# Performance work log

Measured on AMD Instinct MI355X. Metric: run time of the kernel, lower is better.

Reference implementation:

```python
import jax, jax.numpy as jnp
import numpy as np

N = 100000      # nodes
E = 1000000     # edges
D_IN = 64       # in_channels
HID = 64        # hid_channels
ENC = 64        # encoding_dim
OUT = 2         # out_channels (classes)
EDGE_DIM = 32   # TimeEncode dim == edge_dim
HEADS = 2
HD = HID // 2   # per-head channels (32)


def _p(k, shape):
    s = 1.0 / np.sqrt(shape[0])
    return jax.random.uniform(k, shape, jnp.float32, -s, s)


def setup_inputs() -> dict:
    key = jax.random.key(0)
    ks = jax.random.split(key, 40)
    inp = {
        "x": jax.random.normal(ks[0], (N, D_IN), jnp.float32),
        "edge_index": jax.random.randint(ks[1], (2, E), 0, N),
        "node_time": jax.random.uniform(ks[2], (N,), jnp.float32) * 100.0,
        "edge_time": jax.random.uniform(ks[3], (E, 1), jnp.float32) * 100.0,
        "node_mean_out_time_interval": jax.random.uniform(ks[4], (N,), jnp.float32) * 10.0,
        "node_out_degree": jax.random.uniform(ks[5], (N,), jnp.float32) * 50.0,
        "y": jax.random.randint(ks[6], (N,), 0, OUT),
        "train_mask": jnp.ones((N,), bool),
        # TimeEncode: cos(t W + b)
        "time_w": _p(ks[7], (1, EDGE_DIM)), "time_b": jnp.zeros((EDGE_DIM,), jnp.float32),
        # TemporalFrequencyEncoder / DegreeEncoder: Linear(1, ENC)
        "tf_w": _p(ks[8], (1, ENC)), "tf_b": jnp.zeros((ENC,), jnp.float32),
        "deg_w": _p(ks[9], (1, ENC)), "deg_b": jnp.zeros((ENC,), jnp.float32),
        # lin: Linear(in, hid)
        "lin_w": _p(ks[10], (D_IN, HID)), "lin_b": jnp.zeros((HID,), jnp.float32),
        # TransformerConv projections (heads*HD = HID)
        "Wq": _p(ks[11], (HID, HEADS * HD)), "bq": jnp.zeros((HEADS * HD,), jnp.float32),
        "Wk": _p(ks[12], (HID, HEADS * HD)), "bk": jnp.zeros((HEADS * HD,), jnp.float32),
        "Wv": _p(ks[13], (HID, HEADS * HD)), "bv": jnp.zeros((HEADS * HD,), jnp.float32),
        "We": _p(ks[14], (EDGE_DIM, HEADS * HD)), "be": jnp.zeros((HEADS * HD,), jnp.float32),
        "Wskip": _p(ks[15], (HID, HEADS * HD)), "bskip": jnp.zeros((HEADS * HD,), jnp.float32),
        # size-2 context attention
        "wenc_w": _p(ks[16], (ENC, ENC)), "wenc_b": jnp.zeros((ENC,), jnp.float32),
        "wx_w": _p(ks[17], (HID, ENC)), "wx_b": jnp.zeros((ENC,), jnp.float32),
        # lin_combine: Linear(hid+enc, hid)
        "comb_w": _p(ks[18], (HID + ENC, HID)), "comb_b": jnp.zeros((HID,), jnp.float32),
        # out: Linear(hid, out)
        "out_w": _p(ks[19], (HID, OUT)), "out_b": jnp.zeros((OUT,), jnp.float32),
    }
    return inp


def reference(x, edge_index, node_time, edge_time, node_mean_out_time_interval,
              node_out_degree, y, train_mask,
              time_w, time_b, tf_w, tf_b, deg_w, deg_b, lin_w, lin_b,
              Wq, bq, Wk, bk, Wv, bv, We, be, Wskip, bskip,
              wenc_w, wenc_b, wx_w, wx_b, comb_w, comb_b, out_w, out_b):
    src, dst = edge_index[0], edge_index[1]

    # relative edge time -> TimeEncode (cos features), used as edge_attr [E, 32]
    rel_t = node_time[src][:, None] - edge_time          # [E,1]
    rel_t_enc = jnp.cos(rel_t @ time_w + time_b)         # [E,EDGE_DIM]

    h = jax.nn.relu(x @ lin_w + lin_b)                   # [N,HID] (dropout = identity, eval)

    # TransformerConv (PyG math): per-edge attention + scatter-softmax aggregate
    q = (h @ Wq + bq).reshape(N, HEADS, HD)[dst]          # [E,H,HD]
    e = (rel_t_enc @ We + be).reshape(E, HEADS, HD)       # [E,H,HD]
    k = (h @ Wk + bk).reshape(N, HEADS, HD)[src] + e
    v = (h @ Wv + bv).reshape(N, HEADS, HD)[src] + e
    alpha = (q * k).sum(-1) / np.float32(np.sqrt(HD))     # [E,H]
    m = jax.ops.segment_max(alpha, dst, num_segments=N)   # stable softmax per dst node
    ea = jnp.exp(alpha - m[dst])
    denom = jax.ops.segment_sum(ea, dst, num_segments=N)
    a = ea / (denom[dst] + 1e-16)
    agg = jax.ops.segment_sum(a[:, :, None] * v, dst, num_segments=N)
    h1 = agg.reshape(N, HEADS * HD) + h @ Wskip + bskip   # concat heads + root skip

    # size-2 context attention over (temporal-frequency, degree) encodings
    tf_enc = node_mean_out_time_interval[:, None] @ tf_w + tf_b   # [N,ENC]
    deg_enc = node_out_degree[:, None] @ deg_w + deg_b            # [N,ENC]
    enc = jnp.stack((tf_enc, deg_enc), axis=1)                    # [N,2,ENC]
    enc_proj = jnp.tanh(enc @ wenc_w + wenc_b)                    # [N,2,ENC]
    x_proj = jnp.tanh(h1 @ wx_w + wx_b)                           # [N,ENC]
    score = jax.nn.softmax(jnp.einsum('nkd,nd->nk', enc_proj, x_proj), axis=1)  # [N,2]
    context = enc[:, 0] * score[:, 0:1] + enc[:, 1] * score[:, 1:2]

    h1 = jnp.concatenate((h1, context), axis=1) @ comb_w + comb_b  # [N,HID]
    logp = jax.nn.log_softmax(h1 @ out_w + out_b, axis=1)          # [N,OUT]
    return (h1, logp, y, train_mask)
```

## Files before the change

kernel.cpp:

```cpp
#include <hip/hip_runtime.h>
#include <hip/hip_fp16.h>

#define DEV __device__ __forceinline__

typedef _Float16 f16x8 __attribute__((ext_vector_type(8)));
typedef float f32x4 __attribute__((ext_vector_type(4)));

DEV float mask_val(const unsigned char* mb, int n) {
  unsigned b0 = mb[0], b1 = mb[1], b2 = mb[2], b3 = mb[3];
  if (b0 <= 1u && b1 == b0 && b2 == b0 && b3 == b0) {
    return mb[n] ? 1.f : 0.f;
  } else if (b1 == 0u && b2 == 0u && b3 == 0u) {
    return ((const int*)mb)[n] ? 1.f : 0.f;
  } else {
    return (((const float*)mb)[n] != 0.f) ? 1.f : 0.f;
  }
}

DEV float head_sum32(float x) {
  x += __int_as_float(__builtin_amdgcn_ds_swizzle(__float_as_int(x), 0x041F));
  x += __int_as_float(__builtin_amdgcn_ds_swizzle(__float_as_int(x), 0x081F));
  x += __int_as_float(__builtin_amdgcn_ds_swizzle(__float_as_int(x), 0x101F));
  x += __int_as_float(__builtin_amdgcn_ds_swizzle(__float_as_int(x), 0x201F));
  x += __int_as_float(__builtin_amdgcn_ds_swizzle(__float_as_int(x), 0x401F));
  return x;
}

__global__ void k_precompute(const float* __restrict__ tf_w, const float* __restrict__ tf_b,
                             const float* __restrict__ deg_w, const float* __restrict__ deg_b,
                             const float* __restrict__ wenc_w, const float* __restrict__ wenc_b,
                             const float* __restrict__ comb_w, float* __restrict__ cbuf) {
  int c = threadIdx.x;
  float A0 = 0, B0 = 0, A1 = 0, B1 = 0, P0 = 0, Q0 = 0, P1 = 0, Q1 = 0;
  for (int j = 0; j < 64; ++j) {
    float w  = wenc_w[j * 64 + c];
    float cw = comb_w[(64 + j) * 64 + c];
    float twj = tf_w[j], tbj = tf_b[j], dwj = deg_w[j], dbj = deg_b[j];
    A0 += twj * w;  B0 += tbj * w;
    A1 += dwj * w;  B1 += dbj * w;
    P0 += twj * cw; Q0 += tbj * cw;
    P1 += dwj * cw; Q1 += dbj * cw;
  }
  float wb = wenc_b[c];
  cbuf[c]       = A0; cbuf[64 + c]  = B0 + wb;
  cbuf[128 + c] = A1; cbuf[192 + c] = B1 + wb;
  cbuf[256 + c] = P0; cbuf[320 + c] = Q0;
  cbuf[384 + c] = P1; cbuf[448 + c] = Q1;
}

__global__ __launch_bounds__(256) void k_wcvt(
    const float* __restrict__ lin_w, const float* __restrict__ Wq,
    const float* __restrict__ Wk, const float* __restrict__ Wv,
    const float* __restrict__ Wsk, _Float16* __restrict__ wt) {
  const float* Ws[5] = {lin_w, Wq, Wk, Wv, Wsk};
  int idx = blockIdx.x * 256 + threadIdx.x;
  if (idx < 5 * 4096) {
    int s = idx >> 12, r = idx & 4095;
    int j = r >> 6, c = r & 63;
    wt[(s << 12) + c * 64 + j] = (_Float16)Ws[s][j * 64 + c];
  }
}

__global__ __launch_bounds__(256) void k_node_proj(
    const float* __restrict__ x, const _Float16* __restrict__ wt,
    const float* __restrict__ lin_b, const float* __restrict__ bq,
    const float* __restrict__ bk, const float* __restrict__ bv,
    const float* __restrict__ bsk, const float* __restrict__ be,
    float* __restrict__ q, __half2* __restrict__ kvp,
    float* __restrict__ skipout, int N) {
  __shared__ _Float16 H[4][16 * 72];
  const int tid = threadIdx.x;
  const int lane = tid & 63;
  const int wv = tid >> 6;
  const int mrow = lane & 15;
  const int kgrp = lane >> 4;
  const float invs = 0.17677669529663687f;
  float b_lin[4], b_q[4], b_k[4], b_v[4], b_sk[4];
#pragma unroll
  for (int nt = 0; nt < 4; ++nt) {
    const int cc = nt * 16 + mrow;
    b_lin[nt] = lin_b[cc];
    b_q[nt] = bq[cc];
    b_k[nt] = bk[cc] + be[cc];
    b_v[nt] = bv[cc] + be[cc];
    b_sk[nt] = bsk[cc];
  }
  _Float16* Hw = H[wv];
  const int ntiles = (N + 63) >> 6;
  for (int tile = blockIdx.x; tile < ntiles; tile += gridDim.x) {
    const int base = tile << 6;
    const int rowA = base + wv * 16 + mrow;
    const int rclamp = (rowA < N) ? rowA : (N - 1);
    const float* xr = x + (size_t)rclamp * 64 + kgrp * 8;
    const float4 u0 = *(const float4*)xr;
    const float4 u1 = *(const float4*)(xr + 4);
    const float4 u2 = *(const float4*)(xr + 32);
    const float4 u3 = *(const float4*)(xr + 36);
    const f16x8 a0 = {(_Float16)u0.x, (_Float16)u0.y, (_Float16)u0.z, (_Float16)u0.w,
                      (_Float16)u1.x, (_Float16)u1.y, (_Float16)u1.z, (_Float16)u1.w};
    const f16x8 a1 = {(_Float16)u2.x, (_Float16)u2.y, (_Float16)u2.z, (_Float16)u2.w,
                      (_Float16)u3.x, (_Float16)u3.y, (_Float16)u3.z, (_Float16)u3.w};
#pragma unroll
    for (int nt = 0; nt < 4; ++nt) {
      const _Float16* wb0 = wt + (nt * 16 + mrow) * 64 + kgrp * 8;
      const f16x8 B0 = *(const f16x8*)wb0;
      const f16x8 B1 = *(const f16x8*)(wb0 + 32);
      f32x4 C = {0.f, 0.f, 0.f, 0.f};
      C = __builtin_amdgcn_mfma_f32_16x16x32_f16(a0, B0, C, 0, 0, 0);
      C = __builtin_amdgcn_mfma_f32_16x16x32_f16(a1, B1, C, 0, 0, 0);
#pragma unroll
      for (int r = 0; r < 4; ++r) {
        const float hval = fmaxf(C[r] + b_lin[nt], 0.f);
        Hw[(kgrp * 4 + r) * 72 + nt * 16 + mrow] = (_Float16)hval;
      }
    }
    const f16x8 ha0 = *(const f16x8*)(Hw + mrow * 72 + kgrp * 8);
    const f16x8 ha1 = *(const f16x8*)(Hw + mrow * 72 + 32 + kgrp * 8);
    const int orow0 = base + wv * 16 + kgrp * 4;
#pragma unroll
    for (int nt = 0; nt < 4; ++nt) {
      const _Float16* wb0 = wt + 4096 + (nt * 16 + mrow) * 64 + kgrp * 8;
      const f16x8 B0 = *(const f16x8*)wb0;
      const f16x8 B1 = *(const f16x8*)(wb0 + 32);
      f32x4 C = {0.f, 0.f, 0.f, 0.f};
      C = __builtin_amdgcn_mfma_f32_16x16x32_f16(ha0, B0, C, 0, 0, 0);
      C = __builtin_amdgcn_mfma_f32_16x16x32_f16(ha1, B1, C, 0, 0, 0);
#pragma unroll
      for (int r = 0; r < 4; ++r) {
        const int orow = orow0 + r;
        if (orow < N) q[(size_t)orow * 64 + nt * 16 + mrow] = (C[r] + b_q[nt]) * invs;
      }
    }
#pragma unroll
    for (int nt = 0; nt < 4; ++nt) {
      const _Float16* wk0 = wt + 2 * 4096 + (nt * 16 + mrow) * 64 + kgrp * 8;
      const _Float16* wv0 = wt + 3 * 4096 + (nt * 16 + mrow) * 64 + kgrp * 8;
      const f16x8 Bk0 = *(const f16x8*)wk0;
      const f16x8 Bk1 = *(const f16x8*)(wk0 + 32);
      const f16x8 Bv0 = *(const f16x8*)wv0;
      const f16x8 Bv1 = *(const f16x8*)(wv0 + 32);
      f32x4 Ck = {0.f, 0.f, 0.f, 0.f};
      f32x4 Cv = {0.f, 0.f, 0.f, 0.f};
      Ck = __builtin_amdgcn_mfma_f32_16x16x32_f16(ha0, Bk0, Ck, 0, 0, 0);
      Ck = __builtin_amdgcn_mfma_f32_16x16x32_f16(ha1, Bk1, Ck, 0, 0, 0);
      Cv = __builtin_amdgcn_mfma_f32_16x16x32_f16(ha0, Bv0, Cv, 0, 0, 0);
      Cv = __builtin_amdgcn_mfma_f32_16x16x32_f16(ha1, Bv1, Cv, 0, 0, 0);
#pragma unroll
      for (int r = 0; r < 4; ++r) {
        const int orow = orow0 + r;
        if (orow < N)
          kvp[(size_t)orow * 64 + nt * 16 + mrow] =
              __halves2half2(__float2half_rn(Ck[r] + b_k[nt]), __float2half_rn(Cv[r] + b_v[nt]));
      }
    }
#pragma unroll
    for (int nt = 0; nt < 4; ++nt) {
      const _Float16* wb0 = wt + 4 * 4096 + (nt * 16 + mrow) * 64 + kgrp * 8;
      const f16x8 B0 = *(const f16x8*)wb0;
      const f16x8 B1 = *(const f16x8*)(wb0 + 32);
      f32x4 C = {0.f, 0.f, 0.f, 0.f};
      C = __builtin_amdgcn_mfma_f32_16x16x32_f16(ha0, B0, C, 0, 0, 0);
      C = __builtin_amdgcn_mfma_f32_16x16x32_f16(ha1, B1, C, 0, 0, 0);
#pragma unroll
      for (int r = 0; r < 4; ++r) {
        const int orow = orow0 + r;
        if (orow < N) skipout[(size_t)orow * 64 + nt * 16 + mrow] = C[r] + b_sk[nt];
      }
    }
  }
}

__global__ __launch_bounds__(256) void k_hist(const int* __restrict__ ei, int* __restrict__ counts, int E) {
  int i = blockIdx.x * 256 + threadIdx.x;
  if (i < E) atomicAdd(&counts[ei[E + i]], 1);
}

__global__ __launch_bounds__(256) void k_scan1(const int* __restrict__ counts, int* __restrict__ excl,
                                               int* __restrict__ bsum, int N) {
  __shared__ int s[256];
  const int t = threadIdx.x;
  const int idx = blockIdx.x * 256 + t;
  int val = (idx < N) ? counts[idx] : 0;
  s[t] = val;
  __syncthreads();
  for (int d = 1; d < 256; d <<= 1) {
    int add = (t >= d) ? s[t - d] : 0;
    __syncthreads();
    s[t] += add;
    __syncthreads();
  }
  if (idx < N) excl[idx] = s[t] - val;
  if (t == 255) bsum[blockIdx.x] = s[255];
}

__global__ __launch_bounds__(1024) void k_scan2(int* __restrict__ bsum, int B) {
  __shared__ int sm[1024];
  const int t = threadIdx.x;
  if (B <= 1024) {
    int val = (t < B) ? bsum[t] : 0;
    sm[t] = val;
    __syncthreads();
    for (int d = 1; d < 1024; d <<= 1) {
      int add = (t >= d) ? sm[t - d] : 0;
      __syncthreads();
      sm[t] += add;
      __syncthreads();
    }
    if (t < B) bsum[t] = sm[t] - val;
  } else if (t == 0) {
    int acc = 0;
    for (int i = 0; i < B; ++i) { int tt = bsum[i]; bsum[i] = acc; acc += tt; }
  }
}

__global__ __launch_bounds__(256) void k_scan3(const int* __restrict__ bsum, int* __restrict__ rowptr,
                                               int* __restrict__ next, int N, int E) {
  int i = blockIdx.x * 256 + threadIdx.x;
  if (i < N) {
    int r = rowptr[i] + bsum[i >> 8];
    rowptr[i] = r;
    next[i] = r;
  }
  if (i == 0) rowptr[N] = E;
}

__global__ __launch_bounds__(256) void k_fill(const int* __restrict__ ei,
                                              const float* __restrict__ node_time,
                                              const float* __restrict__ edge_time,
                                              int* __restrict__ next, int2* __restrict__ er, int E) {
  int e = blockIdx.x * 256 + threadIdx.x;
  if (e < E) {
    int s = ei[e], d = ei[E + e];
    int pos = atomicAdd(&next[d], 1);
    er[pos] = make_int2(s, __float_as_int(node_time[s] - edge_time[e]));
  }
}

__global__ __launch_bounds__(256) void k_aggregate(
    const int* __restrict__ rowptr, const int2* __restrict__ er,
    const float* __restrict__ q, const unsigned* __restrict__ kvu,
    const float* __restrict__ time_w, const float* __restrict__ time_b,
    const float* __restrict__ We,
    float* __restrict__ h1, int N) {
  __shared__ float swS[4][64];
  const int tid = threadIdx.x;
  const int c = tid & 63;
  const int wv = tid >> 6;
  const float INV2PI = 0.15915494309189535f;
  float wcol[32], Gw[32];
#pragma unroll
  for (int j = 0; j < 32; ++j) wcol[j] = We[j * 64 + c];
#pragma unroll
  for (int j = 0; j < 32; ++j) Gw[j] = We[(c & 31) * 64 + (c & 32) + j];
  const float tw = time_w[c & 31] * INV2PI;
  const float tb = time_b[c & 31] * INV2PI;
  const int h32 = c & 32;
  const int n0 = blockIdx.x * 4 + wv;
  const int nstride = gridDim.x * 4;
  for (int n = n0; n < N; n += nstride) {
    const int start = rowptr[n];
    const int end = rowptr[n + 1];
    const float qc = q[(size_t)n * 64 + c];
    swS[wv][c] = qc;
    float Gc = 0.f;
#pragma unroll
    for (int j = 0; j < 32; ++j) Gc = fmaf(swS[wv][h32 | j], Gw[j], Gc);
    float m = -1e30f, den = 0.f, num = 0.f, S = 0.f;
    for (int ce = start; ce < end; ce += 16) {
      const int cnt = (end - ce < 16) ? (end - ce) : 16;
      int src_[16];
      float rr_[16];
#pragma unroll
      for (int i = 0; i < 16; ++i) {
        const int ee = ce + ((i < cnt) ? i : cnt - 1);
        const int2 a = er[ee];
        src_[i] = a.x;
        rr_[i] = __int_as_float(a.y);
      }
      unsigned kvr[16];
#pragma unroll
      for (int i = 0; i < 16; ++i) kvr[i] = kvu[(size_t)src_[i] * 64 + c];
      float rv_[16], p[16];
#pragma unroll
      for (int i = 0; i < 16; ++i) {
        float ang = fmaf(rr_[i], tw, tb);
        ang = ang - floorf(ang);
        rv_[i] = __builtin_amdgcn_cosf(ang);
        const __half2 h2 = *(const __half2*)&kvr[i];
        p[i] = fmaf(rv_[i], Gc, qc * __half2float(h2.x));
      }
#pragma unroll
      for (int i = 0; i < 16; ++i) p[i] = head_sum32(p[i]);
#pragma unroll
      for (int i = 0; i < 16; ++i)
        if (i >= cnt) p[i] = -1e30f;
      float cm = p[0];
#pragma unroll
      for (int i = 1; i < 16; ++i) cm = fmaxf(cm, p[i]);
      const float mn = fmaxf(m, cm);
      const float sc = __expf(m - mn);
      num *= sc; den *= sc; S *= sc; m = mn;
#pragma unroll
      for (int i = 0; i < 16; ++i) {
        if (i < cnt) {
          const float ea = __expf(p[i] - m);
          const __half2 h2 = *(const __half2*)&kvr[i];
          num = fmaf(ea, __half2float(h2.y), num);
          S = fmaf(ea, rv_[i], S);
          den += ea;
        }
      }
    }
    swS[wv][c] = S;
    float econ = 0.f;
#pragma unroll
    for (int j = 0; j < 32; ++j) econ = fmaf(swS[wv][h32 | j], wcol[j], econ);
    const float agg = (num + econ) / (den + 1e-16f);
    h1[(size_t)n * 64 + c] = agg + h1[(size_t)n * 64 + c];
  }
}

__global__ __launch_bounds__(256) void k_epilogue(
    const float* __restrict__ t_int, const float* __restrict__ deg,
    const float* __restrict__ cbuf,
    const float* __restrict__ wx_w, const float* __restrict__ wx_b,
    const float* __restrict__ comb_w, const float* __restrict__ comb_b,
    const float* __restrict__ out_w, const float* __restrict__ out_b,
    const int* __restrict__ y, const unsigned char* __restrict__ maskb,
    float* __restrict__ out, int N) {
  __shared__ float sh[4][64];
  const int tid = threadIdx.x;
  const int c = tid & 63;
  const int wv = tid >> 6;
  float wxreg[64], cbreg[64];
#pragma unroll
  for (int j = 0; j < 64; ++j) { wxreg[j] = wx_w[j * 64 + c]; cbreg[j] = comb_w[j * 64 + c]; }
  const float A0 = cbuf[c], B0 = cbuf[64 + c], A1 = cbuf[128 + c], B1 = cbuf[192 + c];
  const float P0 = cbuf[256 + c], Q0 = cbuf[320 + c], P1 = cbuf[384 + c], Q1 = cbuf[448 + c];
  const float wxb = wx_b[c], cbb = comb_b[c];
  const float ow0 = out_w[c * 2 + 0], ow1 = out_w[c * 2 + 1];
  const float ob0 = out_b[0], ob1 = out_b[1];
  const size_t O1 = (size_t)N * 64;
  const size_t O2 = O1 + (size_t)N * 2;
  const size_t O3 = O2 + (size_t)N;
  const int ngroups = (N + 3) >> 2;
  for (int g = blockIdx.x; g < ngroups; g += gridDim.x) {
    const int n = g * 4 + wv;
    const bool act = n < N;
    float h1a = 0.f, ti = 0.f, dg = 0.f;
    if (act) {
      h1a = out[(size_t)n * 64 + c];
      ti = t_int[n];
      dg = deg[n];
    }
    sh[wv][c] = h1a;
    __syncthreads();
    const float4* hr = (const float4*)&sh[wv][0];
    float xp = wxb;
    float acc = cbb;
#pragma unroll
    for (int j4 = 0; j4 < 16; ++j4) {
      float4 hv = hr[j4];
      xp  = fmaf(hv.x, wxreg[4 * j4 + 0], xp);
      xp  = fmaf(hv.y, wxreg[4 * j4 + 1], xp);
      xp  = fmaf(hv.z, wxreg[4 * j4 + 2], xp);
      xp  = fmaf(hv.w, wxreg[4 * j4 + 3], xp);
      acc = fmaf(hv.x, cbreg[4 * j4 + 0], acc);
      acc = fmaf(hv.y, cbreg[4 * j4 + 1], acc);
      acc = fmaf(hv.z, cbreg[4 * j4 + 2], acc);
      acc = fmaf(hv.w, cbreg[4 * j4 + 3], acc);
    }
    xp = tanhf(xp);
    const float ep0 = tanhf(fmaf(ti, A0, B0));
    const float ep1 = tanhf(fmaf(dg, A1, B1));
    float d0 = ep0 * xp, d1 = ep1 * xp;
#pragma unroll
    for (int msk = 32; msk >= 1; msk >>= 1) { d0 += __shfl_xor(d0, msk, 64); d1 += __shfl_xor(d1, msk, 64); }
    const float mx = fmaxf(d0, d1);
    const float e0 = expf(d0 - mx), e1 = expf(d1 - mx);
    const float sden = e0 + e1;
    const float s0 = e0 / sden, s1 = e1 / sden;
    acc = fmaf(s0, fmaf(ti, P0, Q0), acc);
    acc = fmaf(s1, fmaf(dg, P1, Q1), acc);
    float z0 = acc * ow0, z1 = acc * ow1;
#pragma unroll
    for (int msk = 32; msk >= 1; msk >>= 1) { z0 += __shfl_xor(z0, msk, 64); z1 += __shfl_xor(z1, msk, 64); }
    if (act) {
      out[(size_t)n * 64 + c] = acc;
      if (c == 0) {
        z0 += ob0; z1 += ob1;
        const float mz = fmaxf(z0, z1);
        const float lse = mz + logf(expf(z0 - mz) + expf(z1 - mz));
        out[O1 + (size_t)n * 2 + 0] = z0 - lse;
        out[O1 + (size_t)n * 2 + 1] = z1 - lse;
        out[O2 + (size_t)n] = (float)y[n];
        out[O3 + (size_t)n] = mask_val(maskb, n);
      }
    }
    __syncthreads();
  }
}

extern "C" void kernel_launch(void* const* d_in, const int* in_sizes, int n_in,
                              void* d_out, int out_size, void* d_ws, size_t ws_size,
                              hipStream_t stream) {
  const float* x          = (const float*)d_in[0];
  const int*   ei         = (const int*)d_in[1];
  const float* node_time  = (const float*)d_in[2];
  const float* edge_time  = (const float*)d_in[3];
  const float* nmoti      = (const float*)d_in[4];
  const float* nod        = (const float*)d_in[5];
  const int*   y          = (const int*)d_in[6];
  const unsigned char* mask = (const unsigned char*)d_in[7];
  const float* time_w = (const float*)d_in[8];
  const float* time_b = (const float*)d_in[9];
  const float* tf_w   = (const float*)d_in[10];
  const float* tf_b   = (const float*)d_in[11];
  const float* deg_w  = (const float*)d_in[12];
  const float* deg_b  = (const float*)d_in[13];
  const float* lin_w  = (const float*)d_in[14];
  const float* lin_b  = (const float*)d_in[15];
  const float* Wq     = (const float*)d_in[16];
  const float* bq     = (const float*)d_in[17];
  const float* Wk     = (const float*)d_in[18];
  const float* bk     = (const float*)d_in[19];
  const float* Wv     = (const float*)d_in[20];
  const float* bv     = (const float*)d_in[21];
  const float* We     = (const float*)d_in[22];
  const float* be     = (const float*)d_in[23];
  const float* Wsk    = (const float*)d_in[24];
  const float* bsk    = (const float*)d_in[25];
  const float* wenc_w = (const float*)d_in[26];
  const float* wenc_b = (const float*)d_in[27];
  const float* wx_w   = (const float*)d_in[28];
  const float* wx_b   = (const float*)d_in[29];
  const float* comb_w = (const float*)d_in[30];
  const float* comb_b = (const float*)d_in[31];
  const float* out_w  = (const float*)d_in[32];
  const float* out_b  = (const float*)d_in[33];

  const int N = in_sizes[2];
  const int E = in_sizes[3];
  const size_t N64 = (size_t)N * 64;

  float*    q    = (float*)d_ws;
  __half2*  kvp  = (__half2*)(q + N64);
  int2*     er   = (int2*)((char*)kvp + N64 * sizeof(__half2));
  int*      counts = (int*)(er + E);
  int*      rowptr = counts + N;
  int*      next   = rowptr + N + 1;
  int*      bsum   = next + N;
  float*    cbuf   = (float*)(bsum + 4096);
  _Float16* wt     = (_Float16*)(cbuf + 512);
  float*    outf   = (float*)d_out;
  float*    skip   = outf;

  const int B = (N + 255) / 256;

  hipMemsetAsync(counts, 0, (size_t)N * sizeof(int), stream);

  k_precompute<<<1, 64, 0, stream>>>(tf_w, tf_b, deg_w, deg_b, wenc_w, wenc_b, comb_w, cbuf);
  k_wcvt<<<80, 256, 0, stream>>>(lin_w, Wq, Wk, Wv, Wsk, wt);

  const int ntiles = (N + 63) >> 6;
  k_node_proj<<<ntiles, 256, 0, stream>>>(x, wt, lin_b, bq, bk, bv, bsk, be,
                                          q, kvp, skip, N);

  const int EB = (E + 255) / 256;
  k_hist<<<EB, 256, 0, stream>>>(ei, counts, E);
  k_scan1<<<B, 256, 0, stream>>>(counts, rowptr, bsum, N);
  k_scan2<<<1, 1024, 0, stream>>>(bsum, B);
  k_scan3<<<B, 256, 0, stream>>>(bsum, rowptr, next, N, E);
  k_fill<<<EB, 256, 0, stream>>>(ei, node_time, edge_time, next, er, E);

  int agb = 768;
  if (agb > (N + 3) / 4) agb = (N + 3) / 4;
  k_aggregate<<<agb, 256, 0, stream>>>(rowptr, er, q, (const unsigned*)kvp,
                                       time_w, time_b, We, outf, N);

  k_epilogue<<<2048, 256, 0, stream>>>(nmoti, nod, cbuf, wx_w, wx_b,
                                       comb_w, comb_b, out_w, out_b, y, mask, outf, N);
}
```

Measured before the change: 414.1 us.

## Compute edge attention scores and aggregation with MFMA via LDS staging

Rewrites the per-chunk attention inner loop in the aggregation kernel. Key/value and time-encoding tiles are staged into per-wave LDS buffers, and both the 16-edge score dot products and the weighted value/time sums are computed with 16x16x32 f16 MFMA instructions. This replaces the swizzle-based 32-lane reductions and scalar exp/FMA loops. It adds LDS traffic and reduced-precision f16 softmax weights, and a 16-edge chunk is wasteful for the average degree of about 10.

```diff
diff --git a/kernel.cpp b/kernel.cpp
--- a/kernel.cpp
+++ b/kernel.cpp
@@ -17,13 +17,13 @@
   }
 }
 
-DEV float head_sum32(float x) {
-  x += __int_as_float(__builtin_amdgcn_ds_swizzle(__float_as_int(x), 0x041F));
-  x += __int_as_float(__builtin_amdgcn_ds_swizzle(__float_as_int(x), 0x081F));
-  x += __int_as_float(__builtin_amdgcn_ds_swizzle(__float_as_int(x), 0x101F));
-  x += __int_as_float(__builtin_amdgcn_ds_swizzle(__float_as_int(x), 0x201F));
-  x += __int_as_float(__builtin_amdgcn_ds_swizzle(__float_as_int(x), 0x401F));
-  return x;
+DEV float swz16(float x) {
+  return __int_as_float(__builtin_amdgcn_ds_swizzle(__float_as_int(x), 0x401F));
+}
+
+DEV unsigned pack_h2(float a, float b) {
+  __half2 t = __halves2half2(__float2half_rn(a), __float2half_rn(b));
+  return *(unsigned*)&t;
 }
 
 __global__ void k_precompute(const float* __restrict__ tf_w, const float* __restrict__ tf_b,
@@ -242,19 +242,42 @@
     const float* __restrict__ time_w, const float* __restrict__ time_b,
     const float* __restrict__ We,
     float* __restrict__ h1, int N) {
+  __shared__ _Float16 KXs[4][16 * 104];
+  __shared__ _Float16 VTs[4][64 * 40];
+  __shared__ _Float16 RVs[4][32 * 40];
+  __shared__ _Float16 QGs[4][128];
+  __shared__ _Float16 EAs[4][64];
   __shared__ float swS[4][64];
   const int tid = threadIdx.x;
-  const int c = tid & 63;
+  const int lane = tid & 63;
   const int wv = tid >> 6;
+  const int c = lane;
+  const int h32 = c & 32;
+  const int mrow = lane & 15;
+  const int koff = (lane >> 4) * 8;
   const float INV2PI = 0.15915494309189535f;
   float wcol[32], Gw[32];
 #pragma unroll
   for (int j = 0; j < 32; ++j) wcol[j] = We[j * 64 + c];
 #pragma unroll
-  for (int j = 0; j < 32; ++j) Gw[j] = We[(c & 31) * 64 + (c & 32) + j];
+  for (int j = 0; j < 32; ++j) Gw[j] = We[(c & 31) * 64 + h32 + j];
   const float tw = time_w[c & 31] * INV2PI;
   const float tb = time_b[c & 31] * INV2PI;
-  const int h32 = c & 32;
+  _Float16* Kx = KXs[wv];
+  _Float16* Vt = VTs[wv];
+  _Float16* Rv = RVs[wv];
+  _Float16* qg = QGs[wv];
+  _Float16* ea = EAs[wv];
+  ea[lane] = (_Float16)0.f;
+  {
+    const uint4 z = make_uint4(0u, 0u, 0u, 0u);
+    *(uint4*)(Vt + lane * 40 + 16) = z;
+    *(uint4*)(Vt + lane * 40 + 24) = z;
+    if (lane < 32) {
+      *(uint4*)(Rv + lane * 40 + 16) = z;
+      *(uint4*)(Rv + lane * 40 + 24) = z;
+    }
+  }
   const int n0 = blockIdx.x * 4 + wv;
   const int nstride = gridDim.x * 4;
   for (int n = n0; n < N; n += nstride) {
@@ -265,51 +288,116 @@
     float Gc = 0.f;
 #pragma unroll
     for (int j = 0; j < 32; ++j) Gc = fmaf(swS[wv][h32 | j], Gw[j], Gc);
-    float m = -1e30f, den = 0.f, num = 0.f, S = 0.f;
+    qg[c] = (_Float16)qc;
+    qg[64 + c] = (_Float16)Gc;
+    const f16x8 qf0 = *(const f16x8*)&qg[koff];
+    const f16x8 qf1 = *(const f16x8*)&qg[32 + koff];
+    const f16x8 gf0 = *(const f16x8*)&qg[64 + koff];
+    const f16x8 gf1 = *(const f16x8*)&qg[96 + koff];
+    float m0 = -1e30f, m1 = -1e30f, num = 0.f, S = 0.f, den = 0.f;
     for (int ce = start; ce < end; ce += 16) {
       const int cnt = (end - ce < 16) ? (end - ce) : 16;
       int src_[16];
-      float rr_[16];
+      float rel_[16];
 #pragma unroll
       for (int i = 0; i < 16; ++i) {
         const int ee = ce + ((i < cnt) ? i : cnt - 1);
         const int2 a = er[ee];
         src_[i] = a.x;
-        rr_[i] = __int_as_float(a.y);
+        rel_[i] = __int_as_float(a.y);
       }
       unsigned kvr[16];
 #pragma unroll
       for (int i = 0; i < 16; ++i) kvr[i] = kvu[(size_t)src_[i] * 64 + c];
-      float rv_[16], p[16];
 #pragma unroll
       for (int i = 0; i < 16; ++i) {
-        float ang = fmaf(rr_[i], tw, tb);
+        union { unsigned short u; _Float16 h; } cv;
+        cv.u = (unsigned short)(kvr[i] & 0xFFFFu);
+        Kx[i * 104 + c] = cv.h;
+      }
+      {
+        unsigned vv[8];
+#pragma unroll
+        for (int j = 0; j < 8; ++j)
+          vv[j] = (kvr[2 * j] >> 16) | (kvr[2 * j + 1] & 0xFFFF0000u);
+        *(uint4*)(Vt + c * 40) = make_uint4(vv[0], vv[1], vv[2], vv[3]);
+        *(uint4*)(Vt + c * 40 + 8) = make_uint4(vv[4], vv[5], vv[6], vv[7]);
+      }
+      float rv_[16];
+#pragma unroll
+      for (int i = 0; i < 16; ++i) {
+        float ang = fmaf(rel_[i], tw, tb);
         ang = ang - floorf(ang);
         rv_[i] = __builtin_amdgcn_cosf(ang);
-        const __half2 h2 = *(const __half2*)&kvr[i];
-        p[i] = fmaf(rv_[i], Gc, qc * __half2float(h2.x));
-      }
-#pragma unroll
-      for (int i = 0; i < 16; ++i) p[i] = head_sum32(p[i]);
-#pragma unroll
-      for (int i = 0; i < 16; ++i)
-        if (i >= cnt) p[i] = -1e30f;
-      float cm = p[0];
-#pragma unroll
-      for (int i = 1; i < 16; ++i) cm = fmaxf(cm, p[i]);
-      const float mn = fmaxf(m, cm);
-      const float sc = __expf(m - mn);
-      num *= sc; den *= sc; S *= sc; m = mn;
-#pragma unroll
-      for (int i = 0; i < 16; ++i) {
-        if (i < cnt) {
-          const float ea = __expf(p[i] - m);
-          const __half2 h2 = *(const __half2*)&kvr[i];
-          num = fmaf(ea, __half2float(h2.y), num);
-          S = fmaf(ea, rv_[i], S);
-          den += ea;
-        }
-      }
+      }
+      if (lane < 32) {
+#pragma unroll
+        for (int i = 0; i < 16; ++i) Kx[i * 104 + 64 + c] = (_Float16)rv_[i];
+        unsigned rr[8];
+#pragma unroll
+        for (int j = 0; j < 8; ++j) rr[j] = pack_h2(rv_[2 * j], rv_[2 * j + 1]);
+        *(uint4*)(Rv + c * 40) = make_uint4(rr[0], rr[1], rr[2], rr[3]);
+        *(uint4*)(Rv + c * 40 + 8) = make_uint4(rr[4], rr[5], rr[6], rr[7]);
+      }
+      const f16x8 Arv = *(const f16x8*)&Kx[mrow * 104 + 64 + koff];
+      const f16x8 Ak0 = *(const f16x8*)&Kx[mrow * 104 + koff];
+      const f16x8 Ak1 = *(const f16x8*)&Kx[mrow * 104 + 32 + koff];
+      f32x4 C0 = {0.f, 0.f, 0.f, 0.f}, C1 = {0.f, 0.f, 0.f, 0.f};
+      C0 = __builtin_amdgcn_mfma_f32_16x16x32_f16(Arv, gf0, C0, 0, 0, 0);
+      C0 = __builtin_amdgcn_mfma_f32_16x16x32_f16(Ak0, qf0, C0, 0, 0, 0);
+      C1 = __builtin_amdgcn_mfma_f32_16x16x32_f16(Arv, gf1, C1, 0, 0, 0);
+      C1 = __builtin_amdgcn_mfma_f32_16x16x32_f16(Ak1, qf1, C1, 0, 0, 0);
+      float x0 = fmaxf(fmaxf(C0[0], C0[1]), fmaxf(C0[2], C0[3]));
+      float x1 = fmaxf(fmaxf(C1[0], C1[1]), fmaxf(C1[2], C1[3]));
+      x0 = fmaxf(x0, swz16(x0)); x0 = fmaxf(x0, __shfl_xor(x0, 32, 64));
+      x1 = fmaxf(x1, swz16(x1)); x1 = fmaxf(x1, __shfl_xor(x1, 32, 64));
+      const float mn0 = fmaxf(m0, x0);
+      const float mn1 = fmaxf(m1, x1);
+      if (mrow < 4) {
+        const int r = lane & 3;
+        const int e = (lane >> 4) * 4 + r;
+        const float p0 = (r == 0) ? C0[0] : (r == 1) ? C0[1] : (r == 2) ? C0[2] : C0[3];
+        const float p1 = (r == 0) ? C1[0] : (r == 1) ? C1[1] : (r == 2) ? C1[2] : C1[3];
+        ea[e] = (_Float16)((e < cnt) ? __expf(p0 - mn0) : 0.f);
+        ea[32 + e] = (_Float16)((e < cnt) ? __expf(p1 - mn1) : 0.f);
+      }
+      float ds0 = 0.f, ds1 = 0.f;
+      const int e0i = (lane >> 4) * 4;
+#pragma unroll
+      for (int r = 0; r < 4; ++r) {
+        const bool ok = (e0i + r) < cnt;
+        ds0 += ok ? __expf(C0[r] - mn0) : 0.f;
+        ds1 += ok ? __expf(C1[r] - mn1) : 0.f;
+      }
+      ds0 += swz16(ds0); ds0 += __shfl_xor(ds0, 32, 64);
+      ds1 += swz16(ds1); ds1 += __shfl_xor(ds1, 32, 64);
+      const float ds = h32 ? ds1 : ds0;
+      const f16x8 eaf0 = *(const f16x8*)&ea[koff];
+      const f16x8 eaf1 = *(const f16x8*)&ea[32 + koff];
+      const f16x8 Bv0 = *(const f16x8*)&Vt[(0 + mrow) * 40 + koff];
+      const f16x8 Bv1 = *(const f16x8*)&Vt[(16 + mrow) * 40 + koff];
+      const f16x8 Bv2 = *(const f16x8*)&Vt[(32 + mrow) * 40 + koff];
+      const f16x8 Bv3 = *(const f16x8*)&Vt[(48 + mrow) * 40 + koff];
+      const f16x8 Br0 = *(const f16x8*)&Rv[(0 + mrow) * 40 + koff];
+      const f16x8 Br1 = *(const f16x8*)&Rv[(16 + mrow) * 40 + koff];
+      const f32x4 Z = {0.f, 0.f, 0.f, 0.f};
+      const f32x4 N0 = __builtin_amdgcn_mfma_f32_16x16x32_f16(eaf0, Bv0, Z, 0, 0, 0);
+      const f32x4 N1 = __builtin_amdgcn_mfma_f32_16x16x32_f16(eaf0, Bv1, Z, 0, 0, 0);
+      const f32x4 N2 = __builtin_amdgcn_mfma_f32_16x16x32_f16(eaf1, Bv2, Z, 0, 0, 0);
+      const f32x4 N3 = __builtin_amdgcn_mfma_f32_16x16x32_f16(eaf1, Bv3, Z, 0, 0, 0);
+      const f32x4 S0 = __builtin_amdgcn_mfma_f32_16x16x32_f16(eaf0, Br0, Z, 0, 0, 0);
+      const f32x4 S1 = __builtin_amdgcn_mfma_f32_16x16x32_f16(eaf0, Br1, Z, 0, 0, 0);
+      const f32x4 S2 = __builtin_amdgcn_mfma_f32_16x16x32_f16(eaf1, Br0, Z, 0, 0, 0);
+      const f32x4 S3 = __builtin_amdgcn_mfma_f32_16x16x32_f16(eaf1, Br1, Z, 0, 0, 0);
+      const int sel = (c >> 4) & 3;
+      const float nadd = (sel == 0) ? N0[0] : (sel == 1) ? N1[0] : (sel == 2) ? N2[0] : N3[0];
+      const float sadd = (sel == 0) ? S0[0] : (sel == 1) ? S1[0] : (sel == 2) ? S2[0] : S3[0];
+      const float sc = __expf((h32 ? m1 : m0) - (h32 ? mn1 : mn0));
+      num = fmaf(num, sc, nadd);
+      S = fmaf(S, sc, sadd);
+      den = fmaf(den, sc, ds);
+      m0 = mn0;
+      m1 = mn1;
     }
     swS[wv][c] = S;
     float econ = 0.f;
```

Measured after the change: 481.5 us. 16.3% more time.

## Software-prefetch next node's first edge chunk in aggregate; drop epilogue block barriers

Applied to the files above, without the earlier changes.

The aggregate kernel now loads the next node's rowptr, edge records and first 16 gathered K/V values while the current node's first chunk is being processed. This hides the dependent gather latency across node iterations. Remaining chunks still use the original loop. The epilogue removes its __syncthreads, since each wavefront only touches its own shared-memory row, and the aggregate grid grows from 768 to 1024 blocks. The prefetch buffers add register pressure, which may reduce occupancy.

```diff
diff --git a/kernel.cpp b/kernel.cpp
--- a/kernel.cpp
+++ b/kernel.cpp
@@ -255,31 +255,62 @@
   const float tw = time_w[c & 31] * INV2PI;
   const float tb = time_b[c & 31] * INV2PI;
   const int h32 = c & 32;
-  const int n0 = blockIdx.x * 4 + wv;
   const int nstride = gridDim.x * 4;
-  for (int n = n0; n < N; n += nstride) {
-    const int start = rowptr[n];
-    const int end = rowptr[n + 1];
+  int n = blockIdx.x * 4 + wv;
+  int pf_start = 0, pf_end = 0;
+  float pf_rr[16];
+  unsigned pf_kvr[16];
+#pragma unroll
+  for (int i = 0; i < 16; ++i) { pf_rr[i] = 0.f; pf_kvr[i] = 0u; }
+  if (n < N) {
+    pf_start = rowptr[n];
+    pf_end = rowptr[n + 1];
+    int pcnt = pf_end - pf_start;
+    if (pcnt > 16) pcnt = 16;
+    if (pcnt > 0) {
+      int psrc[16];
+#pragma unroll
+      for (int i = 0; i < 16; ++i) {
+        const int ee = pf_start + ((i < pcnt) ? i : pcnt - 1);
+        const int2 a = er[ee];
+        psrc[i] = a.x;
+        pf_rr[i] = __int_as_float(a.y);
+      }
+#pragma unroll
+      for (int i = 0; i < 16; ++i) pf_kvr[i] = kvu[(size_t)psrc[i] * 64 + c];
+    }
+  }
+  for (; n < N; n += nstride) {
+    const int start = pf_start, end = pf_end;
+    float rr_[16];
+    unsigned kvr[16];
+#pragma unroll
+    for (int i = 0; i < 16; ++i) { rr_[i] = pf_rr[i]; kvr[i] = pf_kvr[i]; }
+    const int nn = n + nstride;
+    int nstart = 0, nend = 0;
+    if (nn < N) { nstart = rowptr[nn]; nend = rowptr[nn + 1]; }
+    int ncnt = nend - nstart;
+    if (ncnt > 16) ncnt = 16;
+    int nsrc[16];
+    const bool do_pf = (nn < N) && (ncnt > 0);
+    if (do_pf) {
+#pragma unroll
+      for (int i = 0; i < 16; ++i) {
+        const int ee = nstart + ((i < ncnt) ? i : ncnt - 1);
+        const int2 a = er[ee];
+        nsrc[i] = a.x;
+        pf_rr[i] = __int_as_float(a.y);
+      }
+    }
+    const float skipv = h1[(size_t)n * 64 + c];
     const float qc = q[(size_t)n * 64 + c];
     swS[wv][c] = qc;
     float Gc = 0.f;
 #pragma unroll
     for (int j = 0; j < 32; ++j) Gc = fmaf(swS[wv][h32 | j], Gw[j], Gc);
     float m = -1e30f, den = 0.f, num = 0.f, S = 0.f;
-    for (int ce = start; ce < end; ce += 16) {
-      const int cnt = (end - ce < 16) ? (end - ce) : 16;
-      int src_[16];
-      float rr_[16];
-#pragma unroll
-      for (int i = 0; i < 16; ++i) {
-        const int ee = ce + ((i < cnt) ? i : cnt - 1);
-        const int2 a = er[ee];
-        src_[i] = a.x;
-        rr_[i] = __int_as_float(a.y);
-      }
-      unsigned kvr[16];
-#pragma unroll
-      for (int i = 0; i < 16; ++i) kvr[i] = kvu[(size_t)src_[i] * 64 + c];
+    if (end > start) {
+      const int cnt = (end - start < 16) ? (end - start) : 16;
       float rv_[16], p[16];
 #pragma unroll
       for (int i = 0; i < 16; ++i) {
@@ -291,6 +322,10 @@
       }
 #pragma unroll
       for (int i = 0; i < 16; ++i) p[i] = head_sum32(p[i]);
+      if (do_pf) {
+#pragma unroll
+        for (int i = 0; i < 16; ++i) pf_kvr[i] = kvu[(size_t)nsrc[i] * 64 + c];
+      }
 #pragma unroll
       for (int i = 0; i < 16; ++i)
         if (i >= cnt) p[i] = -1e30f;
@@ -310,13 +345,63 @@
           den += ea;
         }
       }
+    } else if (do_pf) {
+#pragma unroll
+      for (int i = 0; i < 16; ++i) pf_kvr[i] = kvu[(size_t)nsrc[i] * 64 + c];
+    }
+    for (int ce = start + 16; ce < end; ce += 16) {
+      const int cnt = (end - ce < 16) ? (end - ce) : 16;
+      int src_t[16];
+      float rr_t[16];
+#pragma unroll
+      for (int i = 0; i < 16; ++i) {
+        const int ee = ce + ((i < cnt) ? i : cnt - 1);
+        const int2 a = er[ee];
+        src_t[i] = a.x;
+        rr_t[i] = __int_as_float(a.y);
+      }
+      unsigned kvr_t[16];
+#pragma unroll
+      for (int i = 0; i < 16; ++i) kvr_t[i] = kvu[(size_t)src_t[i] * 64 + c];
+      float rv_[16], p[16];
+#pragma unroll
+      for (int i = 0; i < 16; ++i) {
+        float ang = fmaf(rr_t[i], tw, tb);
+        ang = ang - floorf(ang);
+        rv_[i] = __builtin_amdgcn_cosf(ang);
+        const __half2 h2 = *(const __half2*)&kvr_t[i];
+        p[i] = fmaf(rv_[i], Gc, qc * __half2float(h2.x));
+      }
+#pragma unroll
+      for (int i = 0; i < 16; ++i) p[i] = head_sum32(p[i]);
+#pragma unroll
+      for (int i = 0; i < 16; ++i)
+        if (i >= cnt) p[i] = -1e30f;
+      float cm = p[0];
+#pragma unroll
+      for (int i = 1; i < 16; ++i) cm = fmaxf(cm, p[i]);
+      const float mn = fmaxf(m, cm);
+      const float sc = __expf(m - mn);
+      num *= sc; den *= sc; S *= sc; m = mn;
+#pragma unroll
+      for (int i = 0; i < 16; ++i) {
+        if (i < cnt) {
+          const float ea = __expf(p[i] - m);
+          const __half2 h2 = *(const __half2*)&kvr_t[i];
+          num = fmaf(ea, __half2float(h2.y), num);
+          S = fmaf(ea, rv_[i], S);
+          den += ea;
+        }
+      }
     }
     swS[wv][c] = S;
     float econ = 0.f;
 #pragma unroll
     for (int j = 0; j < 32; ++j) econ = fmaf(swS[wv][h32 | j], wcol[j], econ);
     const float agg = (num + econ) / (den + 1e-16f);
-    h1[(size_t)n * 64 + c] = agg + h1[(size_t)n * 64 + c];
+    h1[(size_t)n * 64 + c] = agg + skipv;
+    pf_start = nstart;
+    pf_end = nend;
   }
 }
 
@@ -354,7 +439,6 @@
       dg = deg[n];
     }
     sh[wv][c] = h1a;
-    __syncthreads();
     const float4* hr = (const float4*)&sh[wv][0];
     float xp = wxb;
     float acc = cbb;
@@ -397,7 +481,6 @@
         out[O3 + (size_t)n] = mask_val(maskb, n);
       }
     }
-    __syncthreads();
   }
 }
 
@@ -473,7 +556,7 @@
   k_scan3<<<B, 256, 0, stream>>>(bsum, rowptr, next, N, E);
   k_fill<<<EB, 256, 0, stream>>>(ei, node_time, edge_time, next, er, E);
 
-  int agb = 768;
+  int agb = 1024;
   if (agb > (N + 3) / 4) agb = (N + 3) / 4;
   k_aggregate<<<agb, 256, 0, stream>>>(rowptr, er, q, (const unsigned*)kvp,
                                        time_w, time_b, We, outf, N);
```

New measurement: 458.4 us. 10.7% more time.
